# Performance work log

Measured on AMD Instinct MI355X. Metric: run time of the kernel, lower is better.

Reference implementation:

```python
import jax, jax.numpy as jnp
import numpy as np

B, N = 8, 1024
C = [256, 512, 1024]
C2 = C[1]
KV = sum(C)            # 1792
H = 4                  # num_attention_heads
EXPAND = 4
LN_EPS = 1e-6
IN_EPS = 1e-5          # nn.InstanceNorm2d default eps


def setup_inputs() -> dict:
    key = jax.random.key(0)
    ks = jax.random.split(key, 16)
    s = 0.02
    inp = {
        "emb1": jax.random.normal(ks[0], (B, N, C[0]), jnp.float32),
        "emb2": jax.random.normal(ks[1], (B, N, C[1]), jnp.float32),
        "emb3": jax.random.normal(ks[2], (B, N, C[2]), jnp.float32),
        # per-head projection weights stored as [in, out] (torch Linear applies x @ W.T)
        "Wq": jax.random.normal(ks[3], (H, C2, C2), jnp.float32) * s,
        "Wk": jax.random.normal(ks[4], (H, KV, KV), jnp.float32) * s,
        "Wv": jax.random.normal(ks[5], (H, KV, KV), jnp.float32) * s,
        "Wout": jax.random.normal(ks[6], (C2, C2), jnp.float32) * s,
        "ln1_g": jnp.ones((C2,), jnp.float32),
        "ln1_b": jnp.zeros((C2,), jnp.float32),
        "lnall_g": jnp.ones((KV,), jnp.float32),
        "lnall_b": jnp.zeros((KV,), jnp.float32),
        "lnffn_g": jnp.ones((C2,), jnp.float32),
        "lnffn_b": jnp.zeros((C2,), jnp.float32),
        "fc1_w": jax.random.normal(ks[7], (C2, C2 * EXPAND), jnp.float32) * s,
        "fc1_b": jnp.zeros((C2 * EXPAND,), jnp.float32),
        "fc2_w": jax.random.normal(ks[8], (C2 * EXPAND, C2), jnp.float32) * s,
        "fc2_b": jnp.zeros((C2,), jnp.float32),
    }
    return inp


def _layer_norm(x, g, b, eps=LN_EPS):
    m = jnp.mean(x, axis=-1, keepdims=True)
    v = jnp.var(x, axis=-1, keepdims=True)
    return (x - m) * jax.lax.rsqrt(v + eps) * g + b


def _instance_norm2d(x, eps=IN_EPS):
    # x: [B, H, C2, KV]; normalize each (B,H) map over its last two dims (no affine)
    m = jnp.mean(x, axis=(-2, -1), keepdims=True)
    v = jnp.var(x, axis=(-2, -1), keepdims=True)
    return (x - m) * jax.lax.rsqrt(v + eps)


def reference(emb1, emb2, emb3, Wq, Wk, Wv, Wout,
              ln1_g, ln1_b, lnall_g, lnall_b, lnffn_g, lnffn_b,
              fc1_w, fc1_b, fc2_w, fc2_b):
    org2 = emb2
    emb_all = jnp.concatenate([emb1, emb2, emb3], axis=2)        # [B,N,KV]
    cx2 = _layer_norm(emb2, ln1_g, ln1_b)                         # [B,N,C2]
    emb_all = _layer_norm(emb_all, lnall_g, lnall_b)              # [B,N,KV]

    # batched per-head projections (replaces the Python ModuleList loop)
    q = jnp.einsum('bnc,hcd->bhnd', cx2, Wq)                      # [B,H,N,C2]
    k = jnp.einsum('bnc,hcd->bhnd', emb_all, Wk)                  # [B,H,N,KV]
    v = jnp.einsum('bnc,hcd->bhnd', emb_all, Wv)                  # [B,H,N,KV]

    # channel attention: q^T k over the token axis
    scores = jnp.einsum('bhnc,bhnk->bhck', q, k) / np.sqrt(KV)    # [B,H,C2,KV]
    probs = jax.nn.softmax(_instance_norm2d(scores), axis=3)      # [B,H,C2,KV]

    # context = probs @ v^T, then mean over heads (fused into one einsum)
    ctx = jnp.einsum('bhck,bhnk->bnc', probs, v) / H              # [B,N,C2]
    o = ctx @ Wout                                                # [B,N,C2]

    cx2 = org2 + o
    x2 = _layer_norm(cx2, lnffn_g, lnffn_b)
    x2 = jax.nn.gelu(x2 @ fc1_w + fc1_b, approximate=False)
    x2 = x2 @ fc2_w + fc2_b
    return x2 + cx2
```

## Files before the change

### kernel.cpp

```cpp
#include <hip/hip_runtime.h>
#include <cstdint>
#include <cmath>

typedef __bf16 bf16_t;
typedef __attribute__((ext_vector_type(8))) __bf16 bf16x8;
typedef __attribute__((ext_vector_type(4))) float f32x4;

#define AS_G(x) ((__attribute__((address_space(1))) void*)(x))
#define AS_L(x) ((__attribute__((address_space(3))) void*)(x))

#define BK 64

#define BSZ 8
#define NTOK 1024
#define CC2 512
#define KVD 1792
#define NH 4
#define FFD 2048
#define ROWS 8192


__device__ __forceinline__ void stage_pair(const bf16_t* __restrict__ A,
                                           const bf16_t* __restrict__ B,
                                           int ld, bf16_t* ldsA, bf16_t* ldsB, int tid)
{
#pragma unroll
  for (int it = 0; it < 4; ++it) {
    int chunk = it * 256 + tid;
    int r = chunk >> 3;
    int s = chunk & 7;
    int cg = ((s ^ (r & 7)) << 3);
    __builtin_amdgcn_global_load_lds(AS_G(A + (long)r * ld + cg),
                                     AS_L(ldsA + chunk * 8), 16, 0, 0);
    __builtin_amdgcn_global_load_lds(AS_G(B + (long)r * ld + cg),
                                     AS_L(ldsB + chunk * 8), 16, 0, 0);
  }
}

__device__ __forceinline__ void mfma_step(const bf16_t* ldsA, const bf16_t* ldsB,
                                          f32x4 acc[4][4], int wr, int wc, int lane, int kc)
{
  const int quad = lane >> 4, l16 = lane & 15;
  bf16x8 a[4], b[4];
#pragma unroll
  for (int i = 0; i < 4; ++i) {
    int r = wr * 64 + i * 16 + l16;
    int slot = (kc + quad) ^ (r & 7);
    a[i] = *(const bf16x8*)(ldsA + r * BK + slot * 8);
  }
#pragma unroll
  for (int j = 0; j < 4; ++j) {
    int r = wc * 64 + j * 16 + l16;
    int slot = (kc + quad) ^ (r & 7);
    b[j] = *(const bf16x8*)(ldsB + r * BK + slot * 8);
  }
#pragma unroll
  for (int i = 0; i < 4; ++i)
#pragma unroll
    for (int j = 0; j < 4; ++j)
      acc[i][j] = __builtin_amdgcn_mfma_f32_16x16x32_bf16(a[i], b[j], acc[i][j], 0, 0, 0);
}

#define GEMM_PROLOG() \
  __shared__ __align__(16) bf16_t ldsA[128 * BK]; \
  __shared__ __align__(16) bf16_t ldsB[128 * BK]; \
  const int tid = threadIdx.x; \
  const int wave = tid >> 6, lane = tid & 63; \
  const int wr = wave >> 1, wc = wave & 1; \
  f32x4 acc[4][4] = {};

#define GEMM_LOOP(Aptr, Bptr, Kdim) \
  for (int k0 = 0; k0 < (Kdim); k0 += BK) { \
    stage_pair((Aptr) + k0, (Bptr) + k0, (Kdim), ldsA, ldsB, tid); \
    __syncthreads(); \
    mfma_step(ldsA, ldsB, acc, wr, wc, lane, 0); \
    mfma_step(ldsA, ldsB, acc, wr, wc, lane, 4); \
    __syncthreads(); \
  }

template <typename F>
__device__ __forceinline__ void epilogue_apply(f32x4 acc[4][4], int wr, int wc, int lane, F f)
{
  const int quad = lane >> 4, l16 = lane & 15;
#pragma unroll
  for (int i = 0; i < 4; ++i)
#pragma unroll
    for (int j = 0; j < 4; ++j)
#pragma unroll
      for (int r = 0; r < 4; ++r)
        f(wr * 64 + i * 16 + quad * 4 + r, wc * 64 + j * 16 + l16, acc[i][j][r]);
}


__device__ __forceinline__ void stage256(const bf16_t* __restrict__ A,
                                         const bf16_t* __restrict__ B,
                                         int ld, bf16_t* ldsA, bf16_t* ldsB, int tid)
{
#pragma unroll
  for (int it = 0; it < 4; ++it) {
    int chunk = it * 512 + tid;
    int r = chunk >> 3;
    int s = chunk & 7;
    int cg = ((s ^ (r & 7)) << 3);
    __builtin_amdgcn_global_load_lds(AS_G(A + (long)r * ld + cg),
                                     AS_L(ldsA + chunk * 8), 16, 0, 0);
    __builtin_amdgcn_global_load_lds(AS_G(B + (long)r * ld + cg),
                                     AS_L(ldsB + chunk * 8), 16, 0, 0);
  }
}

__device__ __forceinline__ void qread_a(const bf16_t* ldsOp, int wr, int rh, int lane,
                                        bf16x8 a[4][2])
{
  const int quad = lane >> 4, l16 = lane & 15;
#pragma unroll
  for (int mi = 0; mi < 4; ++mi)
#pragma unroll
    for (int kc = 0; kc < 2; ++kc) {
      int r = wr * 128 + rh * 64 + mi * 16 + l16;
      int slot = (kc * 4 + quad) ^ (r & 7);
      a[mi][kc] = *(const bf16x8*)(ldsOp + r * BK + slot * 8);
    }
}

__device__ __forceinline__ void qread_b(const bf16_t* ldsOp, int wc, int ch, int lane,
                                        bf16x8 b[2][2])
{
  const int quad = lane >> 4, l16 = lane & 15;
#pragma unroll
  for (int nj = 0; nj < 2; ++nj)
#pragma unroll
    for (int kc = 0; kc < 2; ++kc) {
      int r = wc * 64 + ch * 32 + nj * 16 + l16;
      int slot = (kc * 4 + quad) ^ (r & 7);
      b[nj][kc] = *(const bf16x8*)(ldsOp + r * BK + slot * 8);
    }
}

template <int RH, int CH, bool TAIL>
__device__ __forceinline__ void phase_mfma(f32x4 acc[8][4], const bf16x8 a[4][2],
                                           const bf16x8 (&b)[2][2])
{
  if (!TAIL) {
    __builtin_amdgcn_s_barrier();
    asm volatile("s_waitcnt lgkmcnt(0)" ::: "memory");
    __builtin_amdgcn_sched_barrier(0);
  }
  __builtin_amdgcn_s_setprio(1);
#pragma unroll
  for (int mi = 0; mi < 4; ++mi)
#pragma unroll
    for (int nj = 0; nj < 2; ++nj)
#pragma unroll
      for (int kc = 0; kc < 2; ++kc)
        acc[RH * 4 + mi][CH * 2 + nj] =
            __builtin_amdgcn_mfma_f32_16x16x32_bf16(a[mi][kc], b[nj][kc],
                                                    acc[RH * 4 + mi][CH * 2 + nj], 0, 0, 0);
  __builtin_amdgcn_s_setprio(0);
  if (TAIL) __syncthreads();
  else __builtin_amdgcn_s_barrier();
}

#define GEMM256_PROLOG() \
  __shared__ __align__(16) bf16_t ldsA[2][256 * BK]; \
  __shared__ __align__(16) bf16_t ldsB[2][256 * BK]; \
  __shared__ float sred[16]; \
  (void)sred; \
  const int tid = threadIdx.x; \
  const int wave = tid >> 6, lane = tid & 63; \
  const int wr = wave >> 2, wc = wave & 3; \
  f32x4 acc[8][4] = {};

#define STAGE256(buf, t) stage256(Ap + (t) * BK, Bp + (t) * BK, Kd, ldsA[buf], ldsB[buf], tid)

#define HALF_TILE(buf) \
    qread_a(ldsA[buf], wr, 0, lane, a); \
    qread_b(ldsB[buf], wc, 0, lane, b[0]); \
    phase_mfma<0, 0, false>(acc, a, b[0]); \
    qread_b(ldsB[buf], wc, 1, lane, b[1]); \
    phase_mfma<0, 1, false>(acc, a, b[1]); \
    qread_a(ldsA[buf], wr, 1, lane, a); \
    phase_mfma<1, 0, false>(acc, a, b[0]); \
    phase_mfma<1, 1, true>(acc, a, b[1]);

#define GEMM256_LOOP(Aptr, Bptr, Kdim) { \
  const bf16_t* Ap = (Aptr); const bf16_t* Bp = (Bptr); const int Kd = (Kdim); \
  const int nit = Kd / (2 * BK); \
  STAGE256(0, 0); \
  __syncthreads(); \
  for (int i = 0; i < nit; ++i) { \
    bf16x8 a[4][2], b[2][2][2]; \
    STAGE256(1, 2 * i + 1); \
    HALF_TILE(0) \
    if (i + 1 < nit) STAGE256(0, 2 * i + 2); \
    HALF_TILE(1) \
  } }

template <typename F>
__device__ __forceinline__ void epi256(f32x4 acc[8][4], int wr, int wc, int lane, F f)
{
  const int quad = lane >> 4, l16 = lane & 15;
#pragma unroll
  for (int i = 0; i < 8; ++i)
#pragma unroll
    for (int j = 0; j < 4; ++j)
#pragma unroll
      for (int r = 0; r < 4; ++r)
        f(wr * 128 + (i >> 2) * 64 + (i & 3) * 16 + quad * 4 + r,
          wc * 64 + (j >> 1) * 32 + (j & 1) * 16 + l16, acc[i][j][r]);
}


__global__ void zstats_k(float* s)
{
  if (threadIdx.x < 64) s[threadIdx.x] = 0.f;
}

__global__ __launch_bounds__(256) void tconv_k(const float* __restrict__ in,
                                               bf16_t* __restrict__ out, int R, int Cc)
{
  __shared__ float tile[32][33];
  const long base = (long)blockIdx.z * R * Cc;
  const int c0 = blockIdx.x * 32, r0 = blockIdx.y * 32;
  const int tx = threadIdx.x & 31, ty = threadIdx.x >> 5;
#pragma unroll
  for (int i = 0; i < 4; ++i)
    tile[ty + i * 8][tx] = in[base + (long)(r0 + ty + i * 8) * Cc + c0 + tx];
  __syncthreads();
#pragma unroll
  for (int i = 0; i < 4; ++i)
    out[base + (long)(c0 + ty + i * 8) * R + r0 + tx] = (bf16_t)tile[tx][ty + i * 8];
}

__global__ __launch_bounds__(256) void tconv_bf_k(const bf16_t* __restrict__ in,
                                                  bf16_t* __restrict__ out, int R, int Cc)
{
  __shared__ float tile[32][33];
  const long base = (long)blockIdx.z * R * Cc;
  const int c0 = blockIdx.x * 32, r0 = blockIdx.y * 32;
  const int tx = threadIdx.x & 31, ty = threadIdx.x >> 5;
#pragma unroll
  for (int i = 0; i < 4; ++i)
    tile[ty + i * 8][tx] = (float)in[base + (long)(r0 + ty + i * 8) * Cc + c0 + tx];
  __syncthreads();
#pragma unroll
  for (int i = 0; i < 4; ++i)
    out[base + (long)(c0 + ty + i * 8) * R + r0 + tx] = (bf16_t)tile[tx][ty + i * 8];
}

__global__ __launch_bounds__(256) void cast_k(const float* __restrict__ in,
                                              bf16_t* __restrict__ out, long n)
{
  long i = ((long)blockIdx.x * 256 + threadIdx.x) * 4;
  if (i + 3 < n) {
    float4 v = *(const float4*)(in + i);
    out[i] = (bf16_t)v.x; out[i + 1] = (bf16_t)v.y;
    out[i + 2] = (bf16_t)v.z; out[i + 3] = (bf16_t)v.w;
  }
}

__global__ __launch_bounds__(256) void msum_add_k(const bf16_t* __restrict__ M,
                                                  bf16_t* __restrict__ O)
{
  long i = ((long)blockIdx.x * 256 + threadIdx.x) * 8;
  bf16x8 x = *(const bf16x8*)(M + i);
  bf16x8 y = *(const bf16x8*)(M + (long)8 * CC2 * KVD + i);
  bf16x8 r;
#pragma unroll
  for (int j = 0; j < 8; ++j) r[j] = (bf16_t)((float)x[j] + (float)y[j]);
  *(bf16x8*)(O + i) = r;
}

__global__ __launch_bounds__(256) void ln_concat_k(const float* __restrict__ e1,
                                                   const float* __restrict__ e2,
                                                   const float* __restrict__ e3,
                                                   const float* __restrict__ g1,
                                                   const float* __restrict__ b1,
                                                   const float* __restrict__ ga,
                                                   const float* __restrict__ ba,
                                                   bf16_t* __restrict__ cxln,
                                                   bf16_t* __restrict__ embln)
{
  const long row = blockIdx.x;
  const float* p1 = e1 + row * 256;
  const float* p2 = e2 + row * 512;
  const float* p3 = e3 + row * 1024;
  const int t = threadIdx.x;
  float vals[7];
  float sa = 0.f, qa = 0.f;
#pragma unroll
  for (int i = 0; i < 7; ++i) {
    int idx = t + i * 256;
    float x = (idx < 256) ? p1[idx] : (idx < 768 ? p2[idx - 256] : p3[idx - 768]);
    vals[i] = x;
    sa += x; qa += x * x;
  }
  float s2 = vals[1] + vals[2];
  float q2 = vals[1] * vals[1] + vals[2] * vals[2];
  for (int off = 32; off; off >>= 1) {
    sa += __shfl_down(sa, off, 64); qa += __shfl_down(qa, off, 64);
    s2 += __shfl_down(s2, off, 64); q2 += __shfl_down(q2, off, 64);
  }
  __shared__ float red[4][4];
  const int wave = t >> 6, lane = t & 63;
  if (lane == 0) { red[0][wave] = sa; red[1][wave] = qa; red[2][wave] = s2; red[3][wave] = q2; }
  __syncthreads();
  float SA = red[0][0] + red[0][1] + red[0][2] + red[0][3];
  float QA = red[1][0] + red[1][1] + red[1][2] + red[1][3];
  float S2 = red[2][0] + red[2][1] + red[2][2] + red[2][3];
  float Q2 = red[3][0] + red[3][1] + red[3][2] + red[3][3];
  float ma = SA * (1.f / 1792.f);
  float va = QA * (1.f / 1792.f) - ma * ma;
  float rsa = rsqrtf(va + 1e-6f);
  float m2 = S2 * (1.f / 512.f);
  float v2 = Q2 * (1.f / 512.f) - m2 * m2;
  float rs2 = rsqrtf(v2 + 1e-6f);
#pragma unroll
  for (int i = 0; i < 7; ++i) {
    int idx = t + i * 256;
    embln[row * 1792 + idx] = (bf16_t)((vals[i] - ma) * rsa * ga[idx] + ba[idx]);
  }
  cxln[row * 512 + t]       = (bf16_t)((vals[1] - m2) * rs2 * g1[t] + b1[t]);
  cxln[row * 512 + t + 256] = (bf16_t)((vals[2] - m2) * rs2 * g1[t + 256] + b1[t + 256]);
}

__global__ __launch_bounds__(256) void ln2_k(const float* __restrict__ X,
                                             const float* __restrict__ g,
                                             const float* __restrict__ bb,
                                             bf16_t* __restrict__ Y)
{
  const long row = blockIdx.x;
  const float* p = X + row * 512;
  const int t = threadIdx.x;
  float x0 = p[t], x1 = p[t + 256];
  float s = x0 + x1, q = x0 * x0 + x1 * x1;
  for (int off = 32; off; off >>= 1) {
    s += __shfl_down(s, off, 64); q += __shfl_down(q, off, 64);
  }
  __shared__ float red[2][4];
  const int wave = t >> 6, lane = t & 63;
  if (lane == 0) { red[0][wave] = s; red[1][wave] = q; }
  __syncthreads();
  float S = red[0][0] + red[0][1] + red[0][2] + red[0][3];
  float Q = red[1][0] + red[1][1] + red[1][2] + red[1][3];
  float m = S * (1.f / 512.f);
  float v = Q * (1.f / 512.f) - m * m;
  float rs = rsqrtf(v + 1e-6f);
  Y[row * 512 + t]       = (bf16_t)((x0 - m) * rs * g[t] + bb[t]);
  Y[row * 512 + t + 256] = (bf16_t)((x1 - m) * rs * g[t + 256] + bb[t + 256]);
}

__global__ __launch_bounds__(256) void softmax_k(bf16_t* __restrict__ SC,
                                                 const float* __restrict__ stats)
{
  const long rowid = blockIdx.x;
  const int z = (int)(rowid >> 9);
  const float inv_cnt = 1.f / (512.f * 1792.f);
  float m = stats[2 * z] * inv_cnt;
  float var = stats[2 * z + 1] * inv_cnt - m * m;
  float rs = rsqrtf(var + 1e-5f);
  bf16_t* rowp = SC + rowid * 1792;
  const int t = threadIdx.x;
  float v[7];
  float mx = -1e30f;
#pragma unroll
  for (int i = 0; i < 7; ++i) {
    v[i] = (float)rowp[t + i * 256] * rs;
    mx = fmaxf(mx, v[i]);
  }
  for (int off = 32; off; off >>= 1) mx = fmaxf(mx, __shfl_down(mx, off, 64));
  __shared__ float red[8];
  const int wave = t >> 6, lane = t & 63;
  if (lane == 0) red[wave] = mx;
  __syncthreads();
  mx = fmaxf(fmaxf(red[0], red[1]), fmaxf(red[2], red[3]));
  float sum = 0.f;
#pragma unroll
  for (int i = 0; i < 7; ++i) { v[i] = __expf(v[i] - mx); sum += v[i]; }
  for (int off = 32; off; off >>= 1) sum += __shfl_down(sum, off, 64);
  if (lane == 0) red[4 + wave] = sum;
  __syncthreads();
  float inv = 1.f / (red[4] + red[5] + red[6] + red[7]);
#pragma unroll
  for (int i = 0; i < 7; ++i) rowp[t + i * 256] = (bf16_t)(v[i] * inv);
}


__global__ __launch_bounds__(256) void gemm_ab(const bf16_t* __restrict__ A, long astride,
                                               const bf16_t* __restrict__ B, long bstride,
                                               bf16_t* __restrict__ C, long cstride,
                                               int K, int ldc)
{
  const int z = blockIdx.z;
  GEMM_PROLOG();
  const bf16_t* Ap = A + z * astride + (long)blockIdx.x * 128 * K;
  const bf16_t* Bp = B + z * bstride + (long)blockIdx.y * 128 * K;
  GEMM_LOOP(Ap, Bp, K);
  bf16_t* Cb = C + (long)z * cstride;
  const int rbase = blockIdx.x * 128, cbase = blockIdx.y * 128;
  epilogue_apply(acc, wr, wc, lane, [&](int rr, int cc, float v) {
    Cb[(long)(rbase + rr) * ldc + cbase + cc] = (bf16_t)v;
  });
}

__global__ __launch_bounds__(512, 2) void gemm_t1_256(const bf16_t* __restrict__ WqT,
                                                      const bf16_t* __restrict__ Gt,
                                                      bf16_t* __restrict__ T1)
{
  const int z = blockIdx.z, hh = z >> 3, b = z & 7;
  GEMM256_PROLOG();
  const bf16_t* Ap0 = WqT + (long)hh * CC2 * CC2 + (long)blockIdx.x * 256 * CC2;
  const bf16_t* Bp0 = Gt + (long)b * KVD * CC2 + (long)blockIdx.y * 256 * CC2;
  GEMM256_LOOP(Ap0, Bp0, CC2);
  bf16_t* Cb = T1 + (long)z * CC2 * KVD;
  const int rbase = blockIdx.x * 256, cbase = blockIdx.y * 256;
  epi256(acc, wr, wc, lane, [&](int rr, int cc, float v) {
    Cb[(long)(rbase + rr) * KVD + cbase + cc] = (bf16_t)v;
  });
}

__global__ __launch_bounds__(512, 2) void gemm_scores_256(const bf16_t* __restrict__ T1,
                                                          const bf16_t* __restrict__ WkT,
                                                          bf16_t* __restrict__ SC,
                                                          float* __restrict__ stats)
{
  const int z = blockIdx.z, hh = z >> 3;
  GEMM256_PROLOG();
  const bf16_t* Ap0 = T1 + (long)z * CC2 * KVD + (long)blockIdx.x * 256 * KVD;
  const bf16_t* Bp0 = WkT + (long)hh * KVD * KVD + (long)blockIdx.y * 256 * KVD;
  GEMM256_LOOP(Ap0, Bp0, KVD);
  const float scale = 0.02362277854f;
  bf16_t* Cb = SC + (long)z * CC2 * KVD;
  const int rbase = blockIdx.x * 256, cbase = blockIdx.y * 256;
  float s = 0.f, q = 0.f;
  epi256(acc, wr, wc, lane, [&](int rr, int cc, float v) {
    v *= scale;
    Cb[(long)(rbase + rr) * KVD + cbase + cc] = (bf16_t)v;
    s += v; q += v * v;
  });
  for (int off = 32; off; off >>= 1) { s += __shfl_down(s, off, 64); q += __shfl_down(q, off, 64); }
  if (lane == 0) { sred[wave] = s; sred[8 + wave] = q; }
  __syncthreads();
  if (tid == 0) {
    float S = 0.f, Q = 0.f;
#pragma unroll
    for (int w = 0; w < 8; ++w) { S += sred[w]; Q += sred[8 + w]; }
    atomicAdd(&stats[2 * z], S);
    atomicAdd(&stats[2 * z + 1], Q);
  }
}

__global__ __launch_bounds__(512, 2) void gemm_macc_256(const bf16_t* __restrict__ P,
                                                        const bf16_t* __restrict__ WvB,
                                                        bf16_t* __restrict__ M, int first)
{
  const int z = blockIdx.z, hh = z >> 3;
  GEMM256_PROLOG();
  const bf16_t* Ap0 = P + (long)z * CC2 * KVD + (long)blockIdx.x * 256 * KVD;
  const bf16_t* Bp0 = WvB + (long)hh * KVD * KVD + (long)blockIdx.y * 256 * KVD;
  GEMM256_LOOP(Ap0, Bp0, KVD);
  bf16_t* Cb = M + (long)z * CC2 * KVD;
  const int rbase = blockIdx.x * 256, cbase = blockIdx.y * 256;
  epi256(acc, wr, wc, lane, [&](int rr, int cc, float v) {
    long idx = (long)(rbase + rr) * KVD + cbase + cc;
    float prev = first ? 0.f : (float)Cb[idx];
    Cb[idx] = (bf16_t)(prev + v * 0.25f);
  });
}

__global__ __launch_bounds__(256) void gemm_ctx(const bf16_t* __restrict__ E,
                                                const bf16_t* __restrict__ Msum8,
                                                bf16_t* __restrict__ CTX)
{
  const int b = blockIdx.z;
  GEMM_PROLOG();
  const bf16_t* Ap = E + (long)b * NTOK * KVD + (long)blockIdx.x * 128 * KVD;
  const bf16_t* Bp = Msum8 + (long)b * CC2 * KVD + (long)blockIdx.y * 128 * KVD;
  GEMM_LOOP(Ap, Bp, KVD);
  bf16_t* Cb = CTX + (long)b * NTOK * CC2;
  const int rbase = blockIdx.x * 128, cbase = blockIdx.y * 128;
  epilogue_apply(acc, wr, wc, lane, [&](int rr, int cc, float v) {
    Cb[(long)(rbase + rr) * CC2 + cbase + cc] = (bf16_t)v;
  });
}

__global__ __launch_bounds__(256) void gemm_resid(const bf16_t* __restrict__ A,
                                                  const bf16_t* __restrict__ B,
                                                  const float* __restrict__ emb2,
                                                  float* __restrict__ CX2)
{
  GEMM_PROLOG();
  const bf16_t* Ap = A + (long)blockIdx.x * 128 * CC2;
  const bf16_t* Bp = B + (long)blockIdx.y * 128 * CC2;
  GEMM_LOOP(Ap, Bp, CC2);
  const int rbase = blockIdx.x * 128, cbase = blockIdx.y * 128;
  epilogue_apply(acc, wr, wc, lane, [&](int rr, int cc, float v) {
    long idx = (long)(rbase + rr) * CC2 + cbase + cc;
    CX2[idx] = v + emb2[idx];
  });
}

__global__ __launch_bounds__(512, 2) void gemm_gelu_256(const bf16_t* __restrict__ A,
                                                        const bf16_t* __restrict__ B,
                                                        const float* __restrict__ bias,
                                                        bf16_t* __restrict__ H)
{
  GEMM256_PROLOG();
  const bf16_t* Ap0 = A + (long)blockIdx.x * 256 * CC2;
  const bf16_t* Bp0 = B + (long)blockIdx.y * 256 * CC2;
  GEMM256_LOOP(Ap0, Bp0, CC2);
  const int rbase = blockIdx.x * 256, cbase = blockIdx.y * 256;
  epi256(acc, wr, wc, lane, [&](int rr, int cc, float v) {
    float x = v + bias[cbase + cc];
    float g = 0.5f * x * (1.0f + erff(x * 0.70710678118f));
    H[(long)(rbase + rr) * FFD + cbase + cc] = (bf16_t)g;
  });
}

__global__ __launch_bounds__(256) void gemm_out(const bf16_t* __restrict__ A,
                                                const bf16_t* __restrict__ B,
                                                const float* __restrict__ bias,
                                                const float* __restrict__ CX2,
                                                float* __restrict__ OUT)
{
  GEMM_PROLOG();
  const bf16_t* Ap = A + (long)blockIdx.x * 128 * FFD;
  const bf16_t* Bp = B + (long)blockIdx.y * 128 * FFD;
  GEMM_LOOP(Ap, Bp, FFD);
  const int rbase = blockIdx.x * 128, cbase = blockIdx.y * 128;
  epilogue_apply(acc, wr, wc, lane, [&](int rr, int cc, float v) {
    long idx = (long)(rbase + rr) * CC2 + cbase + cc;
    OUT[idx] = v + bias[cbase + cc] + CX2[idx];
  });
}


extern "C" void kernel_launch(void* const* d_in, const int* in_sizes, int n_in,
                              void* d_out, int out_size, void* d_ws, size_t ws_size,
                              hipStream_t stream)
{
  const float* emb1   = (const float*)d_in[0];
  const float* emb2   = (const float*)d_in[1];
  const float* emb3   = (const float*)d_in[2];
  const float* Wq     = (const float*)d_in[3];
  const float* Wk     = (const float*)d_in[4];
  const float* Wv     = (const float*)d_in[5];
  const float* Wout   = (const float*)d_in[6];
  const float* ln1_g  = (const float*)d_in[7];
  const float* ln1_b  = (const float*)d_in[8];
  const float* lnall_g = (const float*)d_in[9];
  const float* lnall_b = (const float*)d_in[10];
  const float* lnffn_g = (const float*)d_in[11];
  const float* lnffn_b = (const float*)d_in[12];
  const float* fc1_w  = (const float*)d_in[13];
  const float* fc1_b  = (const float*)d_in[14];
  const float* fc2_w  = (const float*)d_in[15];
  const float* fc2_b  = (const float*)d_in[16];
  float* out = (float*)d_out;

  char* ws = (char*)d_ws;
  size_t off = 0;
  auto alloc = [&](size_t bytes) {
    size_t r = off;
    off = (off + bytes + 255) & ~(size_t)255;
    return r;
  };

  size_t oEMBLN = alloc((size_t)ROWS * KVD * 2);
  size_t oCXLN  = alloc((size_t)ROWS * CC2 * 2);
  size_t oCX2   = alloc((size_t)ROWS * CC2 * 4);
  size_t oGt    = alloc((size_t)BSZ * KVD * CC2 * 2);
  size_t oMsum  = alloc((size_t)16 * CC2 * KVD * 2);
  size_t oWOT   = alloc((size_t)CC2 * CC2 * 2);
  size_t oF1T   = alloc((size_t)FFD * CC2 * 2);
  size_t oF2T   = alloc((size_t)CC2 * FFD * 2);
  size_t oSTATS = alloc(64 * 4);
  size_t oSCR   = alloc(0);
  size_t oCXLNT  = alloc((size_t)BSZ * CC2 * NTOK * 2);
  size_t oEMBLNT = alloc((size_t)BSZ * KVD * NTOK * 2);
  (void)ws_size; (void)in_sizes; (void)n_in; (void)out_size;

  bf16_t* EMBLN  = (bf16_t*)(ws + oEMBLN);
  bf16_t* CXLN   = (bf16_t*)(ws + oCXLN);
  float*  CX2    = (float*)(ws + oCX2);
  bf16_t* Gt     = (bf16_t*)(ws + oGt);
  bf16_t* Msum   = (bf16_t*)(ws + oMsum);
  bf16_t* WOT    = (bf16_t*)(ws + oWOT);
  bf16_t* F1T    = (bf16_t*)(ws + oF1T);
  bf16_t* F2T    = (bf16_t*)(ws + oF2T);
  float*  STATS  = (float*)(ws + oSTATS);
  bf16_t* CXLNT  = (bf16_t*)(ws + oCXLNT);
  bf16_t* EMBLNT = (bf16_t*)(ws + oEMBLNT);
  char* scr = ws + oSCR;
  auto rnd = [](size_t v) { return (v + 255) & ~(size_t)255; };
  bf16_t* WqT = (bf16_t*)(scr);
  bf16_t* WkT = (bf16_t*)(scr + rnd((size_t)2 * CC2 * CC2 * 2));
  bf16_t* WvB = (bf16_t*)((char*)WkT + rnd((size_t)2 * KVD * KVD * 2));
  bf16_t* T1  = (bf16_t*)((char*)WvB + rnd((size_t)2 * KVD * KVD * 2));
  bf16_t* SC  = (bf16_t*)((char*)T1 + rnd((size_t)16 * CC2 * KVD * 2));
  bf16_t* Msum8 = (bf16_t*)(scr);
  bf16_t* CTX   = (bf16_t*)(scr + rnd((size_t)8 * CC2 * KVD * 2));
  bf16_t* FFNH  = (bf16_t*)((char*)CTX + rnd((size_t)ROWS * CC2 * 2));
  bf16_t* X2LN = CXLN;

  zstats_k<<<1, 64, 0, stream>>>(STATS);
  tconv_k<<<dim3(16, 16), 256, 0, stream>>>(Wout, WOT, 512, 512);
  tconv_k<<<dim3(64, 16), 256, 0, stream>>>(fc1_w, F1T, 512, 2048);
  tconv_k<<<dim3(16, 64), 256, 0, stream>>>(fc2_w, F2T, 2048, 512);

  ln_concat_k<<<8192, 256, 0, stream>>>(emb1, emb2, emb3, ln1_g, ln1_b,
                                        lnall_g, lnall_b, CXLN, EMBLN);

  tconv_bf_k<<<dim3(16, 32, 8), 256, 0, stream>>>(CXLN, CXLNT, 1024, 512);
  tconv_bf_k<<<dim3(56, 32, 8), 256, 0, stream>>>(EMBLN, EMBLNT, 1024, 1792);
  gemm_ab<<<dim3(14, 4, 8), 256, 0, stream>>>(EMBLNT, (long)KVD * NTOK,
                                              CXLNT, (long)CC2 * NTOK,
                                              Gt, (long)KVD * CC2, NTOK, CC2);

  for (int g = 0; g < 2; ++g) {
    tconv_k<<<dim3(16, 16, 2), 256, 0, stream>>>(Wq + (long)g * 2 * CC2 * CC2, WqT, 512, 512);
    tconv_k<<<dim3(56, 56, 2), 256, 0, stream>>>(Wk + (long)g * 2 * KVD * KVD, WkT, 1792, 1792);
    cast_k<<<6272, 256, 0, stream>>>(Wv + (long)g * 2 * KVD * KVD, WvB, (long)2 * KVD * KVD);

    gemm_t1_256<<<dim3(2, 7, 16), 512, 0, stream>>>(WqT, Gt, T1);
    gemm_scores_256<<<dim3(2, 7, 16), 512, 0, stream>>>(T1, WkT, SC, STATS + g * 32);
    softmax_k<<<8192, 256, 0, stream>>>(SC, STATS + g * 32);
    gemm_macc_256<<<dim3(2, 7, 16), 512, 0, stream>>>(SC, WvB, Msum, g == 0 ? 1 : 0);
  }

  msum_add_k<<<3584, 256, 0, stream>>>(Msum, Msum8);
  gemm_ctx<<<dim3(8, 4, 8), 256, 0, stream>>>(EMBLN, Msum8, CTX);

  gemm_resid<<<dim3(64, 4), 256, 0, stream>>>(CTX, WOT, emb2, CX2);

  ln2_k<<<8192, 256, 0, stream>>>(CX2, lnffn_g, lnffn_b, X2LN);
  gemm_gelu_256<<<dim3(32, 8), 512, 0, stream>>>(X2LN, F1T, fc1_b, FFNH);
  gemm_out<<<dim3(64, 4), 256, 0, stream>>>(FFNH, F2T, fc2_b, CX2, out);
}
```

Baseline: 791.0 us.

## Double-buffer LDS in GEMM loops with vmcnt waits and XCD-aware block swizzle

The 128-tile GEMM loop now keeps two LDS buffers and prefetches the next K tile while computing the current one, waiting with explicit vmcnt counts instead of full __syncthreads. The 256-tile loop is restructured into a single per-tile pipeline with explicit barriers and lgkmcnt waits around each MFMA phase. A block-index swizzle maps the 224 blocks of the three big GEMMs so that blocks sharing a head and weight panel land on the same XCD, aiming for better L2 reuse. The 128-tile kernels double their LDS footprint, which may reduce occupancy, and the swizzle hardcodes a 2x7x16 grid.

```diff
diff --git a/kernel.cpp b/kernel.cpp
--- a/kernel.cpp
+++ b/kernel.cpp
@@ -18,6 +18,12 @@
 #define NH 4
 #define FFD 2048
 #define ROWS 8192
+
+#define BARM()   asm volatile("s_barrier" ::: "memory")
+#define VMCNT8() asm volatile("s_waitcnt vmcnt(8)" ::: "memory")
+#define VMCNT0() asm volatile("s_waitcnt vmcnt(0)" ::: "memory")
+#define LGKM0()  do { asm volatile("s_waitcnt lgkmcnt(0)" ::: "memory"); \
+                      __builtin_amdgcn_sched_barrier(0); } while (0)
 
 
 __device__ __forceinline__ void stage_pair(const bf16_t* __restrict__ A,
@@ -62,21 +68,28 @@
 }
 
 #define GEMM_PROLOG() \
-  __shared__ __align__(16) bf16_t ldsA[128 * BK]; \
-  __shared__ __align__(16) bf16_t ldsB[128 * BK]; \
+  __shared__ __align__(16) bf16_t ldsA[2][128 * BK]; \
+  __shared__ __align__(16) bf16_t ldsB[2][128 * BK]; \
   const int tid = threadIdx.x; \
   const int wave = tid >> 6, lane = tid & 63; \
   const int wr = wave >> 1, wc = wave & 1; \
   f32x4 acc[4][4] = {};
 
-#define GEMM_LOOP(Aptr, Bptr, Kdim) \
-  for (int k0 = 0; k0 < (Kdim); k0 += BK) { \
-    stage_pair((Aptr) + k0, (Bptr) + k0, (Kdim), ldsA, ldsB, tid); \
-    __syncthreads(); \
-    mfma_step(ldsA, ldsB, acc, wr, wc, lane, 0); \
-    mfma_step(ldsA, ldsB, acc, wr, wc, lane, 4); \
-    __syncthreads(); \
-  }
+#define GEMM_LOOP(Aptr, Bptr, Kdim) { \
+  const bf16_t* Ap_ = (Aptr); const bf16_t* Bp_ = (Bptr); const int Kd_ = (Kdim); \
+  const int nt_ = Kd_ / BK; \
+  stage_pair(Ap_, Bp_, Kd_, ldsA[0], ldsB[0], tid); \
+  for (int t = 0; t < nt_; ++t) { \
+    const int cur = t & 1; \
+    if (t + 1 < nt_) { \
+      stage_pair(Ap_ + (t + 1) * BK, Bp_ + (t + 1) * BK, Kd_, ldsA[cur ^ 1], ldsB[cur ^ 1], tid); \
+      VMCNT8(); \
+    } else { VMCNT0(); } \
+    BARM(); \
+    mfma_step(ldsA[cur], ldsB[cur], acc, wr, wc, lane, 0); \
+    mfma_step(ldsA[cur], ldsB[cur], acc, wr, wc, lane, 4); \
+    BARM(); \
+  } }
 
 template <typename F>
 __device__ __forceinline__ void epilogue_apply(f32x4 acc[4][4], int wr, int wc, int lane, F f)
@@ -137,16 +150,10 @@
     }
 }
 
-template <int RH, int CH, bool TAIL>
-__device__ __forceinline__ void phase_mfma(f32x4 acc[8][4], const bf16x8 a[4][2],
-                                           const bf16x8 (&b)[2][2])
-{
-  if (!TAIL) {
-    __builtin_amdgcn_s_barrier();
-    asm volatile("s_waitcnt lgkmcnt(0)" ::: "memory");
-    __builtin_amdgcn_sched_barrier(0);
-  }
-  __builtin_amdgcn_s_setprio(1);
+template <int RH, int CH>
+__device__ __forceinline__ void mfma16(f32x4 acc[8][4], const bf16x8 a[4][2],
+                                       const bf16x8 (&b)[2][2])
+{
 #pragma unroll
   for (int mi = 0; mi < 4; ++mi)
 #pragma unroll
@@ -156,9 +163,6 @@
         acc[RH * 4 + mi][CH * 2 + nj] =
             __builtin_amdgcn_mfma_f32_16x16x32_bf16(a[mi][kc], b[nj][kc],
                                                     acc[RH * 4 + mi][CH * 2 + nj], 0, 0, 0);
-  __builtin_amdgcn_s_setprio(0);
-  if (TAIL) __syncthreads();
-  else __builtin_amdgcn_s_barrier();
 }
 
 #define GEMM256_PROLOG() \
@@ -171,29 +175,32 @@
   const int wr = wave >> 2, wc = wave & 3; \
   f32x4 acc[8][4] = {};
 
-#define STAGE256(buf, t) stage256(Ap + (t) * BK, Bp + (t) * BK, Kd, ldsA[buf], ldsB[buf], tid)
-
-#define HALF_TILE(buf) \
-    qread_a(ldsA[buf], wr, 0, lane, a); \
-    qread_b(ldsB[buf], wc, 0, lane, b[0]); \
-    phase_mfma<0, 0, false>(acc, a, b[0]); \
-    qread_b(ldsB[buf], wc, 1, lane, b[1]); \
-    phase_mfma<0, 1, false>(acc, a, b[1]); \
-    qread_a(ldsA[buf], wr, 1, lane, a); \
-    phase_mfma<1, 0, false>(acc, a, b[0]); \
-    phase_mfma<1, 1, true>(acc, a, b[1]);
-
 #define GEMM256_LOOP(Aptr, Bptr, Kdim) { \
   const bf16_t* Ap = (Aptr); const bf16_t* Bp = (Bptr); const int Kd = (Kdim); \
-  const int nit = Kd / (2 * BK); \
-  STAGE256(0, 0); \
-  __syncthreads(); \
-  for (int i = 0; i < nit; ++i) { \
-    bf16x8 a[4][2], b[2][2][2]; \
-    STAGE256(1, 2 * i + 1); \
-    HALF_TILE(0) \
-    if (i + 1 < nit) STAGE256(0, 2 * i + 2); \
-    HALF_TILE(1) \
+  const int nt = Kd / BK; \
+  stage256(Ap, Bp, Kd, ldsA[0], ldsB[0], tid); \
+  bf16x8 a[4][2], b0[2][2], b1[2][2]; \
+  for (int t = 0; t < nt; ++t) { \
+    const int cur = t & 1; \
+    if (t + 1 < nt) { \
+      stage256(Ap + (t + 1) * BK, Bp + (t + 1) * BK, Kd, ldsA[cur ^ 1], ldsB[cur ^ 1], tid); \
+      VMCNT8(); \
+    } else { VMCNT0(); } \
+    BARM(); \
+    qread_a(ldsA[cur], wr, 0, lane, a); \
+    qread_b(ldsB[cur], wc, 0, lane, b0); \
+    LGKM0(); \
+    __builtin_amdgcn_s_setprio(1); mfma16<0, 0>(acc, a, b0); __builtin_amdgcn_s_setprio(0); \
+    BARM(); \
+    qread_b(ldsB[cur], wc, 1, lane, b1); \
+    LGKM0(); \
+    __builtin_amdgcn_s_setprio(1); mfma16<0, 1>(acc, a, b1); __builtin_amdgcn_s_setprio(0); \
+    BARM(); \
+    qread_a(ldsA[cur], wr, 1, lane, a); \
+    LGKM0(); \
+    __builtin_amdgcn_s_setprio(1); mfma16<1, 0>(acc, a, b0); __builtin_amdgcn_s_setprio(0); \
+    BARM(); \
+    __builtin_amdgcn_s_setprio(1); mfma16<1, 1>(acc, a, b1); __builtin_amdgcn_s_setprio(0); \
   } }
 
 template <typename F>
@@ -208,6 +215,17 @@
       for (int r = 0; r < 4; ++r)
         f(wr * 128 + (i >> 2) * 64 + (i & 3) * 16 + quad * 4 + r,
           wc * 64 + (j >> 1) * 32 + (j & 1) * 16 + l16, acc[i][j][r]);
+}
+
+__device__ __forceinline__ void swz224(int& bx, int& by, int& bz)
+{
+  int lid = blockIdx.x + 2 * (blockIdx.y + 7 * blockIdx.z);
+  int xcd = lid & 7, s = lid >> 3;
+  int hh = xcd >> 2, bp = xcd & 3;
+  int y = s % 7, t2 = s / 7;
+  bx = t2 & 1;
+  by = y;
+  bz = hh * 8 + bp * 2 + (t2 >> 1);
 }
 
 
@@ -407,13 +425,15 @@
                                                       const bf16_t* __restrict__ Gt,
                                                       bf16_t* __restrict__ T1)
 {
-  const int z = blockIdx.z, hh = z >> 3, b = z & 7;
+  int bxx, byy, bzz;
+  swz224(bxx, byy, bzz);
+  const int z = bzz, hh = z >> 3, b = z & 7;
   GEMM256_PROLOG();
-  const bf16_t* Ap0 = WqT + (long)hh * CC2 * CC2 + (long)blockIdx.x * 256 * CC2;
-  const bf16_t* Bp0 = Gt + (long)b * KVD * CC2 + (long)blockIdx.y * 256 * CC2;
+  const bf16_t* Ap0 = WqT + (long)hh * CC2 * CC2 + (long)bxx * 256 * CC2;
+  const bf16_t* Bp0 = Gt + (long)b * KVD * CC2 + (long)byy * 256 * CC2;
   GEMM256_LOOP(Ap0, Bp0, CC2);
   bf16_t* Cb = T1 + (long)z * CC2 * KVD;
-  const int rbase = blockIdx.x * 256, cbase = blockIdx.y * 256;
+  const int rbase = bxx * 256, cbase = byy * 256;
   epi256(acc, wr, wc, lane, [&](int rr, int cc, float v) {
     Cb[(long)(rbase + rr) * KVD + cbase + cc] = (bf16_t)v;
   });
@@ -424,14 +444,16 @@
                                                           bf16_t* __restrict__ SC,
                                                           float* __restrict__ stats)
 {
-  const int z = blockIdx.z, hh = z >> 3;
+  int bxx, byy, bzz;
+  swz224(bxx, byy, bzz);
+  const int z = bzz, hh = z >> 3;
   GEMM256_PROLOG();
-  const bf16_t* Ap0 = T1 + (long)z * CC2 * KVD + (long)blockIdx.x * 256 * KVD;
-  const bf16_t* Bp0 = WkT + (long)hh * KVD * KVD + (long)blockIdx.y * 256 * KVD;
+  const bf16_t* Ap0 = T1 + (long)z * CC2 * KVD + (long)bxx * 256 * KVD;
+  const bf16_t* Bp0 = WkT + (long)hh * KVD * KVD + (long)byy * 256 * KVD;
   GEMM256_LOOP(Ap0, Bp0, KVD);
   const float scale = 0.02362277854f;
   bf16_t* Cb = SC + (long)z * CC2 * KVD;
-  const int rbase = blockIdx.x * 256, cbase = blockIdx.y * 256;
+  const int rbase = bxx * 256, cbase = byy * 256;
   float s = 0.f, q = 0.f;
   epi256(acc, wr, wc, lane, [&](int rr, int cc, float v) {
     v *= scale;
@@ -454,13 +476,15 @@
                                                         const bf16_t* __restrict__ WvB,
                                                         bf16_t* __restrict__ M, int first)
 {
-  const int z = blockIdx.z, hh = z >> 3;
+  int bxx, byy, bzz;
+  swz224(bxx, byy, bzz);
+  const int z = bzz, hh = z >> 3;
   GEMM256_PROLOG();
-  const bf16_t* Ap0 = P + (long)z * CC2 * KVD + (long)blockIdx.x * 256 * KVD;
-  const bf16_t* Bp0 = WvB + (long)hh * KVD * KVD + (long)blockIdx.y * 256 * KVD;
+  const bf16_t* Ap0 = P + (long)z * CC2 * KVD + (long)bxx * 256 * KVD;
+  const bf16_t* Bp0 = WvB + (long)hh * KVD * KVD + (long)byy * 256 * KVD;
   GEMM256_LOOP(Ap0, Bp0, KVD);
   bf16_t* Cb = M + (long)z * CC2 * KVD;
-  const int rbase = blockIdx.x * 256, cbase = blockIdx.y * 256;
+  const int rbase = bxx * 256, cbase = byy * 256;
   epi256(acc, wr, wc, lane, [&](int rr, int cc, float v) {
     long idx = (long)(rbase + rr) * KVD + cbase + cc;
     float prev = first ? 0.f : (float)Cb[idx];
```

After: 779.8 us. No clear change (-1.4%).
